# Performance work log

Measured on AMD Instinct MI355X. Metric: run time of the kernel, lower is better.

## Reference

```python
import jax, jax.numpy as jnp
import numpy as np

# Static problem dims (match input_specs / init_kwargs)
B, NQ, C, H = 2, 900, 256, 8
HGT, WID = 64, 64            # single-scale feature map (input_spatial_shapes = [[64, 64]])
N = HGT * WID                # 4096 keys
DH = C // H                  # head dim 32
RPE_HID = 512
STRIDE = 16                  # feature_stride


def setup_inputs() -> dict:
    key = jax.random.key(0)
    ks = jax.random.split(key, 24)
    p = lambda k, shape: jax.random.normal(k, shape, jnp.float32) * 0.02
    # reference boxes (cx, cy, w, h) in pixel coords of a 1024x1024 image
    ref = jax.random.uniform(ks[0], (B, NQ, 1, 4), jnp.float32)
    ref = jnp.concatenate([ref[..., :2] * (WID * STRIDE), ref[..., 2:] * 128.0], axis=-1)
    return {
        "vggt_features": jnp.zeros((1,), jnp.float32),  # unused by forward (kept for signature fidelity)
        "query": jax.random.normal(ks[1], (B, NQ, C), jnp.float32),
        "reference_2d": ref,
        "k_input_flatten": jax.random.normal(ks[2], (B, N, C), jnp.float32),
        "v_input_flatten": jax.random.normal(ks[3], (B, N, C), jnp.float32),
        "input_spatial_shapes": jnp.array([[HGT, WID]], jnp.int32),
        "input_padding_mask": jnp.zeros((B, N), jnp.bool_),
        # cpb_mlp1 (x) and cpb_mlp2 (y): Linear(2,512)+ReLU+Linear(512,H,no bias); stored as [in,out]
        "W1x": p(ks[4], (2, RPE_HID)), "b1x": jnp.zeros((RPE_HID,), jnp.float32), "W2x": p(ks[5], (RPE_HID, H)),
        "W1y": p(ks[6], (2, RPE_HID)), "b1y": jnp.zeros((RPE_HID,), jnp.float32), "W2y": p(ks[7], (RPE_HID, H)),
        "Wq": p(ks[8], (C, C)), "bq": jnp.zeros((C,), jnp.float32),
        "Wk": p(ks[9], (C, C)), "bk": jnp.zeros((C,), jnp.float32),
        "Wv": p(ks[10], (C, C)), "bv": jnp.zeros((C,), jnp.float32),
        "Wp": p(ks[11], (C, C)), "bp": jnp.zeros((C,), jnp.float32),
    }


def _mlp(d, W1, b1, W2):
    return jax.nn.relu(d @ W1 + b1) @ W2


def reference(vggt_features, query, reference_2d, k_input_flatten, v_input_flatten,
              input_spatial_shapes, input_padding_mask,
              W1x, b1x, W2x, W1y, b1y, W2y, Wq, bq, Wk, bk, Wv, bv, Wp, bp):
    h, w = HGT, WID  # static (input_spatial_shapes[0] == [HGT, WID])
    scale = DH ** -0.5
    # cxcywh -> xyxy: [B, NQ, 1, 4]
    xyxy = jnp.concatenate([reference_2d[..., :2] - reference_2d[..., 2:] / 2,
                            reference_2d[..., :2] + reference_2d[..., 2:] / 2], axis=-1)
    # pixel-center grid coords (linspace(0.5, w-0.5, w) * stride)
    pos_x = ((jnp.arange(w, dtype=jnp.float32) + 0.5) * STRIDE)[None, None, :, None]
    pos_y = ((jnp.arange(h, dtype=jnp.float32) + 0.5) * STRIDE)[None, None, :, None]
    delta_x = xyxy[..., 0::2] - pos_x  # [B, NQ, w, 2]  (x1, x2 rel. to columns)
    delta_y = xyxy[..., 1::2] - pos_y  # [B, NQ, h, 2]  (y1, y2 rel. to rows)
    rpe_x = _mlp(delta_x, W1x, b1x, W2x)  # [B, NQ, w, H]
    rpe_y = _mlp(delta_y, W1y, b1y, W2y)  # [B, NQ, h, H]
    # broadcast add over (row, col) then flatten spatial -> [B, H, NQ, N]
    rpe = (rpe_x[:, :, None] + rpe_y[:, :, :, None]).reshape(B, NQ, h * w, H).transpose(0, 3, 1, 2)
    q = (query @ Wq + bq).reshape(B, NQ, H, DH).transpose(0, 2, 1, 3) * scale  # [B,H,NQ,DH]
    k = (k_input_flatten @ Wk + bk).reshape(B, N, H, DH).transpose(0, 2, 1, 3)  # [B,H,N,DH]
    v = (v_input_flatten @ Wv + bv).reshape(B, N, H, DH).transpose(0, 2, 1, 3)  # [B,H,N,DH]
    attn = jnp.einsum('bhqd,bhkd->bhqk', q, k) + rpe
    attn = attn + input_padding_mask[:, None, None, :].astype(attn.dtype) * (-100.0)
    # torch.clip_ to finfo(min,max) is an identity on finite values; softmax follows
    attn = jax.nn.softmax(attn, axis=-1)
    x = jnp.einsum('bhqk,bhkd->bhqd', attn, v).transpose(0, 2, 1, 3).reshape(B, NQ, C)
    return x @ Wp + bp
```

## Files before the change

### kernel.cpp

```cpp
#include <hip/hip_runtime.h>
#include <hip/hip_bf16.h>
#include <cmath>

#define B_ 2
#define NQ_ 900
#define N_ 4096
#define LOG2E 1.4426950408889634f

typedef __attribute__((ext_vector_type(4))) float f32x4;
typedef __attribute__((ext_vector_type(8))) short s16x8;
typedef __attribute__((ext_vector_type(8))) _Float16 f16x8;

__device__ inline short f2bf(float x) {
    union { __hip_bfloat16 b; short s; } u;
    u.b = __float2bfloat16(x);
    return u.s;
}
__device__ inline short f2h(float x) {
    _Float16 h = (_Float16)x;
    return __builtin_bit_cast(short, h);
}

template <int CTRL>
__device__ inline float dppf(float x) {
    int xi = __builtin_bit_cast(int, x);
    int r = __builtin_amdgcn_update_dpp(xi, xi, CTRL, 0xF, 0xF, true);
    return __builtin_bit_cast(float, r);
}
__device__ inline float rowmax16(float v) {
    v = fmaxf(v, dppf<0x121>(v));
    v = fmaxf(v, dppf<0x122>(v));
    v = fmaxf(v, dppf<0x124>(v));
    v = fmaxf(v, dppf<0x128>(v));
    return v;
}
__device__ inline float rowsum16(float v) {
    v += dppf<0x121>(v);
    v += dppf<0x122>(v);
    v += dppf<0x124>(v);
    v += dppf<0x128>(v);
    return v;
}

__global__ __launch_bounds__(256) void stage1_kernel(
    const float* __restrict__ query, const float* __restrict__ kin,
    const float* __restrict__ vin,
    const float* __restrict__ Wq, const float* __restrict__ Wk,
    const float* __restrict__ Wv,
    const float* __restrict__ bqv, const float* __restrict__ bkv,
    const float* __restrict__ bvv,
    unsigned short* __restrict__ qbf, unsigned short* __restrict__ kbf,
    unsigned short* __restrict__ vbf, float qscale,
    const float* __restrict__ ref2d,
    const float* __restrict__ W1x, const float* __restrict__ b1x,
    const float* __restrict__ W1y, const float* __restrict__ b1y,
    const float* __restrict__ W2x, const float* __restrict__ W2y,
    float* __restrict__ rpe_x, float* __restrict__ rpe_y)
{
    __shared__ uint4 smem[2560];
    const int bx = blockIdx.x;
    const int tid = threadIdx.x;
    const int w = tid >> 6, l = tid & 63, quad = l >> 4, l15 = l & 15;

    if (bx < 285) {
        short* Bb = (short*)smem;
        const int mtx = bx < 29 ? 0 : (bx < 157 ? 1 : 2);
        const int tile = bx - (mtx == 0 ? 0 : mtx == 1 ? 29 : 157);
        const int m0 = tile * 64;
        const float* X = mtx == 0 ? query : mtx == 1 ? kin : vin;
        const float* W = mtx == 0 ? Wq : mtx == 1 ? Wk : Wv;
        const float* bias = mtx == 0 ? bqv : mtx == 1 ? bkv : bvv;
        unsigned short* Y = mtx == 0 ? qbf : mtx == 1 ? kbf : vbf;
        const int M = mtx == 0 ? 1800 : 8192;
        const float alpha = mtx == 0 ? qscale : 1.0f;
        const int rows_per_b = mtx == 0 ? 900 : 4096;
        const int ROWS = mtx == 0 ? 960 : 4096;
        const int wq = tid & 3, mm = tid >> 2;

        s16x8 afr[8];
        {
            const int arow = m0 + w * 16 + l15;
            const bool avalid = arow < M;
            const float* xr = X + (size_t)arow * 256;
            #pragma unroll
            for (int kc = 0; kc < 8; ++kc) {
                float4 a0 = make_float4(0.f, 0.f, 0.f, 0.f), a1 = a0;
                if (avalid) {
                    a0 = *(const float4*)(xr + kc * 32 + quad * 8);
                    a1 = *(const float4*)(xr + kc * 32 + quad * 8 + 4);
                }
                unsigned pk0 = (unsigned)(unsigned short)f2bf(a0.x) | ((unsigned)(unsigned short)f2bf(a0.y) << 16);
                unsigned pk1 = (unsigned)(unsigned short)f2bf(a0.z) | ((unsigned)(unsigned short)f2bf(a0.w) << 16);
                unsigned pk2 = (unsigned)(unsigned short)f2bf(a1.x) | ((unsigned)(unsigned short)f2bf(a1.y) << 16);
                unsigned pk3 = (unsigned)(unsigned short)f2bf(a1.z) | ((unsigned)(unsigned short)f2bf(a1.w) << 16);
                uint4 pk = make_uint4(pk0, pk1, pk2, pk3);
                afr[kc] = __builtin_bit_cast(s16x8, pk);
            }
        }

        for (int nt0 = 0; nt0 < 4; ++nt0) {
            const int n0 = nt0 * 64;
            {
                const float* wcol = W + n0 + mm;
                #pragma unroll
                for (int it = 0; it < 8; ++it) {
                    int g2 = it * 4 + wq;
                    uint4 wk4;
                    wk4.x = (unsigned)(unsigned short)f2bf(wcol[(g2 * 8 + 0) * 256])
                          | ((unsigned)(unsigned short)f2bf(wcol[(g2 * 8 + 1) * 256]) << 16);
                    wk4.y = (unsigned)(unsigned short)f2bf(wcol[(g2 * 8 + 2) * 256])
                          | ((unsigned)(unsigned short)f2bf(wcol[(g2 * 8 + 3) * 256]) << 16);
                    wk4.z = (unsigned)(unsigned short)f2bf(wcol[(g2 * 8 + 4) * 256])
                          | ((unsigned)(unsigned short)f2bf(wcol[(g2 * 8 + 5) * 256]) << 16);
                    wk4.w = (unsigned)(unsigned short)f2bf(wcol[(g2 * 8 + 6) * 256])
                          | ((unsigned)(unsigned short)f2bf(wcol[(g2 * 8 + 7) * 256]) << 16);
                    *(uint4*)(Bb + (it * 256 + mm * 4 + wq) * 8) = wk4;
                }
            }
            __syncthreads();

            f32x4 acc[4] = {{0.f,0.f,0.f,0.f},{0.f,0.f,0.f,0.f},{0.f,0.f,0.f,0.f},{0.f,0.f,0.f,0.f}};
            #pragma unroll
            for (int kc = 0; kc < 8; ++kc) {
                #pragma unroll
                for (int nt = 0; nt < 4; ++nt) {
                    s16x8 bf = *(const s16x8*)(Bb + (kc * 256 + (nt * 16 + l15) * 4 + quad) * 8);
                    acc[nt] = __builtin_amdgcn_mfma_f32_16x16x32_bf16(afr[kc], bf, acc[nt], 0, 0, 0);
                }
            }

            #pragma unroll
            for (int nt = 0; nt < 4; ++nt) {
                int n = n0 + nt * 16 + l15;
                float bs = bias[n];
                int h = n >> 5, d = n & 31;
                #pragma unroll
                for (int r = 0; r < 4; ++r) {
                    int row = m0 + w * 16 + quad * 4 + r;
                    if (row < M) {
                        int b = row / rows_per_b;
                        int pos = row - b * rows_per_b;
                        Y[((size_t)(b * 8 + h) * ROWS + pos) * 32 + d] =
                            (unsigned short)f2bf((acc[nt][r] + bs) * alpha);
                    }
                }
            }
            __syncthreads();
        }
    } else {
        short* sw2h = (short*)smem;
        short* sw2l = (short*)smem + 8192;
        float4* sUV = (float4*)(smem + 2048);
        const int bq0 = (bx - 285) * 4;

        for (int i = tid; i < 8192; i += 256) {
            int g = i >> 3, j = i & 7;
            int kcg = g >> 6, rr = g & 63, n = rr >> 2, q4 = rr & 3;
            int k = kcg * 32 + q4 * 8 + j;
            float val = ((n < 8) ? W2x[k * 8 + n] : W2y[k * 8 + (n - 8)]) * LOG2E;
            _Float16 hi = (_Float16)val;
            sw2h[i] = __builtin_bit_cast(short, hi);
            sw2l[i] = f2h(val - (float)hi);
        }

        const int k0 = tid, k1 = tid + 256;
        const float w1x0a = W1x[k0], w1x1a = W1x[512 + k0];
        const float w1y0a = W1y[k0], w1y1a = W1y[512 + k0];
        const float bxa = b1x[k0], bya = b1y[k0];
        const float vxa = -(w1x0a + w1x1a), vya = -(w1y0a + w1y1a);
        const float w1x0b = W1x[k1], w1x1b = W1x[512 + k1];
        const float w1y0b = W1y[k1], w1y1b = W1y[512 + k1];
        const float bxb = b1x[k1], byb = b1y[k1];
        const float vxb = -(w1x0b + w1x1b), vyb = -(w1y0b + w1y1b);

        const int wrow = w;
        const int row = wrow * 16 + l15;
        const float pc = (row + 0.5f) * 16.0f;

        for (int qi = 0; qi < 4; ++qi) {
            const int bq = bq0 + qi;
            {
                const float4 bb = *(const float4*)(ref2d + (size_t)bq * 4);
                float x1 = bb.x - bb.z * 0.5f, x2 = bb.x + bb.z * 0.5f;
                float y1 = bb.y - bb.w * 0.5f, y2 = bb.y + bb.w * 0.5f;
                sUV[k0] = make_float4(fmaf(w1x0a, x1, fmaf(w1x1a, x2, bxa)), vxa,
                                      fmaf(w1y0a, y1, fmaf(w1y1a, y2, bya)), vya);
                sUV[k1] = make_float4(fmaf(w1x0b, x1, fmaf(w1x1b, x2, bxb)), vxb,
                                      fmaf(w1y0b, y1, fmaf(w1y1b, y2, byb)), vyb);
            }
            __syncthreads();

            f32x4 accx = {0.f, 0.f, 0.f, 0.f}, accy = {0.f, 0.f, 0.f, 0.f};
            for (int kc = 0; kc < 16; ++kc) {
                f16x8 axh, axl, ayh, ayl;
                #pragma unroll
                for (int i = 0; i < 8; ++i) {
                    float4 u = sUV[kc * 32 + quad * 8 + i];
                    float hx = fmaxf(fmaf(u.y, pc, u.x), 0.f);
                    float hy = fmaxf(fmaf(u.w, pc, u.z), 0.f);
                    _Float16 xh = (_Float16)hx;
                    _Float16 yh = (_Float16)hy;
                    axh[i] = xh;
                    axl[i] = (_Float16)(hx - (float)xh);
                    ayh[i] = yh;
                    ayl[i] = (_Float16)(hy - (float)yh);
                }
                f16x8 bh = *(const f16x8*)(sw2h + (kc * 64 + l15 * 4 + quad) * 8);
                f16x8 bl = *(const f16x8*)(sw2l + (kc * 64 + l15 * 4 + quad) * 8);
                accx = __builtin_amdgcn_mfma_f32_16x16x32_f16(axh, bh, accx, 0, 0, 0);
                accx = __builtin_amdgcn_mfma_f32_16x16x32_f16(axh, bl, accx, 0, 0, 0);
                accx = __builtin_amdgcn_mfma_f32_16x16x32_f16(axl, bh, accx, 0, 0, 0);
                accy = __builtin_amdgcn_mfma_f32_16x16x32_f16(ayh, bh, accy, 0, 0, 0);
                accy = __builtin_amdgcn_mfma_f32_16x16x32_f16(ayh, bl, accy, 0, 0, 0);
                accy = __builtin_amdgcn_mfma_f32_16x16x32_f16(ayl, bh, accy, 0, 0, 0);
            }

            #pragma unroll
            for (int rr = 0; rr < 4; ++rr) {
                int row_out = wrow * 16 + quad * 4 + rr;
                if (l15 < 8) rpe_x[((size_t)l15 * 1800 + bq) * 64 + row_out] = accx[rr];
                else         rpe_y[((size_t)(l15 - 8) * 1800 + bq) * 64 + row_out] = accy[rr];
            }
            __syncthreads();
        }
    }
}

__global__ __launch_bounds__(256) void outproj_kernel(
    const float* __restrict__ X, const float* __restrict__ W,
    const float* __restrict__ bias, float* __restrict__ Y, int M)
{
    __shared__ short Abh[4096], Abl[4096], Bbh[4096], Bbl[4096];
    const int tid = threadIdx.x;
    const int m0 = blockIdx.x * 64, n0 = blockIdx.y * 64;
    const int w = tid >> 6, l = tid & 63, quad = l >> 4, l15 = l & 15;
    const int wq = tid & 3, mm = tid >> 2;
    const bool valid = (m0 + mm) < M;
    const float* xr = X + (size_t)(m0 + mm) * 256;
    const float* wcol = W + n0 + mm;

    f32x4 acc[4] = {{0.f,0.f,0.f,0.f},{0.f,0.f,0.f,0.f},{0.f,0.f,0.f,0.f},{0.f,0.f,0.f,0.f}};

    for (int kq = 0; kq < 4; ++kq) {
        #pragma unroll
        for (int it = 0; it < 2; ++it) {
            int g2 = it * 4 + wq;
            int kbase = kq * 64 + g2 * 8;
            float av[8], bv[8];
            #pragma unroll
            for (int j = 0; j < 8; ++j) {
                av[j] = valid ? xr[kbase + j] : 0.f;
                bv[j] = wcol[(kbase + j) * 256];
            }
            uint4 ah, al, bh, bl;
            unsigned* ahp = (unsigned*)&ah; unsigned* alp = (unsigned*)&al;
            unsigned* bhp = (unsigned*)&bh; unsigned* blp = (unsigned*)&bl;
            #pragma unroll
            for (int j2 = 0; j2 < 4; ++j2) {
                _Float16 h0 = (_Float16)av[j2 * 2], h1 = (_Float16)av[j2 * 2 + 1];
                ahp[j2] = (unsigned)(unsigned short)__builtin_bit_cast(short, h0)
                        | ((unsigned)(unsigned short)__builtin_bit_cast(short, h1) << 16);
                alp[j2] = (unsigned)(unsigned short)f2h(av[j2 * 2] - (float)h0)
                        | ((unsigned)(unsigned short)f2h(av[j2 * 2 + 1] - (float)h1) << 16);
                _Float16 g0 = (_Float16)bv[j2 * 2], g1 = (_Float16)bv[j2 * 2 + 1];
                bhp[j2] = (unsigned)(unsigned short)__builtin_bit_cast(short, g0)
                        | ((unsigned)(unsigned short)__builtin_bit_cast(short, g1) << 16);
                blp[j2] = (unsigned)(unsigned short)f2h(bv[j2 * 2] - (float)g0)
                        | ((unsigned)(unsigned short)f2h(bv[j2 * 2 + 1] - (float)g1) << 16);
            }
            int gi = (it * 256 + mm * 4 + wq) * 8;
            *(uint4*)(Abh + gi) = ah;
            *(uint4*)(Abl + gi) = al;
            *(uint4*)(Bbh + gi) = bh;
            *(uint4*)(Bbl + gi) = bl;
        }
        __syncthreads();

        #pragma unroll
        for (int kc = 0; kc < 2; ++kc) {
            int ga = (kc * 256 + (w * 16 + l15) * 4 + quad) * 8;
            f16x8 ah = *(const f16x8*)(Abh + ga);
            f16x8 al = *(const f16x8*)(Abl + ga);
            #pragma unroll
            for (int nt = 0; nt < 4; ++nt) {
                int gb = (kc * 256 + (nt * 16 + l15) * 4 + quad) * 8;
                f16x8 bh = *(const f16x8*)(Bbh + gb);
                f16x8 bl = *(const f16x8*)(Bbl + gb);
                acc[nt] = __builtin_amdgcn_mfma_f32_16x16x32_f16(ah, bh, acc[nt], 0, 0, 0);
                acc[nt] = __builtin_amdgcn_mfma_f32_16x16x32_f16(ah, bl, acc[nt], 0, 0, 0);
                acc[nt] = __builtin_amdgcn_mfma_f32_16x16x32_f16(al, bh, acc[nt], 0, 0, 0);
            }
        }
        __syncthreads();
    }

    #pragma unroll
    for (int nt = 0; nt < 4; ++nt) {
        int n = n0 + nt * 16 + l15;
        float bs = bias[n];
        #pragma unroll
        for (int r = 0; r < 4; ++r) {
            int row = m0 + w * 16 + quad * 4 + r;
            if (row < M)
                Y[(size_t)row * 256 + n] = acc[nt][r] + bs;
        }
    }
}

__global__ __launch_bounds__(512, 4) void attn_mfma_kernel(
    const unsigned short* __restrict__ qb16, const unsigned short* __restrict__ kb16,
    const unsigned short* __restrict__ vb16,
    const float* __restrict__ rpe_x, const float* __restrict__ rpe_y,
    const unsigned char* __restrict__ mask, float* __restrict__ xout)
{
    __shared__ short skf[4 * 2048];
    __shared__ short svt[4 * 2048];
    __shared__ short spb[8 * 544];
    __shared__ float ry[32 * 65];
    __shared__ unsigned long long smaskb[64];
    __shared__ float sm[8][16], sl[8][16], sLf[32];

    const int tid = threadIdx.x;
    const int qb = blockIdx.x, h = blockIdx.y, b = blockIdx.z;
    const int q0 = qb * 32;
    const int w = tid >> 6, l = tid & 63;
    const int qsub = w >> 2, g = w & 3;
    const int quad = l >> 4, l15 = l & 15;

    const unsigned short* qg = qb16 + (size_t)(b * 8 + h) * 960 * 32;
    const unsigned short* kg = kb16 + (size_t)(b * 8 + h) * 4096 * 32;
    const unsigned short* vg = vb16 + (size_t)(b * 8 + h) * 4096 * 32;
    const float* rxh = rpe_x + ((size_t)h * 1800 + b * NQ_) * 64;
    const float* ryh = rpe_y + ((size_t)h * 1800 + b * NQ_) * 64;

    for (int i = tid; i < 2048; i += 512) {
        int qq = q0 + (i >> 6), pos = i & 63;
        float vy = 0.f;
        if (qq < NQ_)
            vy = ryh[(size_t)qq * 64 + pos];
        ry[(i >> 6) * 65 + pos] = vy;
    }
    #pragma unroll
    for (int j = 0; j < 8; ++j) {
        int c = w * 8 + j;
        unsigned long long bits = __ballot(mask[(size_t)b * N_ + c * 64 + l] != 0);
        if (l == 0) smaskb[c] = bits;
    }

    s16x8 qa = *(const s16x8*)(qg + (size_t)(q0 + qsub * 16 + l15) * 32 + quad * 8);

    f32x4 rx4[4];
    #pragma unroll
    for (int t = 0; t < 4; ++t)
        #pragma unroll
        for (int r = 0; r < 4; ++r) {
            int qq = q0 + qsub * 16 + quad * 4 + r;
            rx4[t][r] = (qq < NQ_) ? rxh[(size_t)qq * 64 + t * 16 + l15] : 0.f;
        }

    const int sg = tid >> 7, role = (tid >> 6) & 1, stl = tid & 63;
    int eoff[4];
    if (role == 0) {
        #pragma unroll
        for (int t = 0; t < 4; ++t)
            eoff[t] = (t * 16 + (stl & 15)) * 32 + (stl >> 4) * 8;
    } else {
        #pragma unroll
        for (int t = 0; t < 4; ++t)
            eoff[t] = stl * 32 + t * 8;
    }
    const unsigned short* src = role ? vg : kg;

    uint4 pf[4];
    {
        size_t cb = (size_t)(sg * 16) * 2048;
        #pragma unroll
        for (int t = 0; t < 4; ++t) pf[t] = *(const uint4*)(src + cb + eoff[t]);
    }

    float mrow[4] = {-INFINITY, -INFINITY, -INFINITY, -INFINITY};
    float lrow[4] = {0.f, 0.f, 0.f, 0.f};
    f32x4 acc0 = {0.f, 0.f, 0.f, 0.f}, acc1 = {0.f, 0.f, 0.f, 0.f};
    short* pw = spb + w * 544;

    for (int i = 0; i < 16; ++i) {
        __syncthreads();
        if (role == 0) {
            #pragma unroll
            for (int t = 0; t < 4; ++t)
                *(uint4*)(skf + sg * 2048 + (t * 64 + stl) * 8) = pf[t];
        } else {
            short* vtw = svt + sg * 2048;
            #pragma unroll
            for (int t = 0; t < 4; ++t) {
                const unsigned short* pv = (const unsigned short*)&pf[t];
                #pragma unroll
                for (int j = 0; j < 8; ++j) {
                    int d = t * 8 + j;
                    vtw[d * 64 + (((stl >> 3) ^ (d & 7)) << 3) + (stl & 7)] = (short)pv[j];
                }
            }
        }
        __syncthreads();

        {
            int inext = (i + 1 < 16) ? i + 1 : 15;
            size_t cb = (size_t)(sg * 16 + inext) * 2048;
            #pragma unroll
            for (int t = 0; t < 4; ++t) pf[t] = *(const uint4*)(src + cb + eoff[t]);
        }

        const int cgc = g * 16 + i;
        const short* kf = skf + g * 2048;

        f32x4 sc[4];
        #pragma unroll
        for (int t = 0; t < 4; ++t) {
            s16x8 kb = *(const s16x8*)(kf + (t * 64 + l) * 8);
            sc[t] = __builtin_amdgcn_mfma_f32_16x16x32_bf16(qa, kb, rx4[t], 0, 0, 0);
        }
        float ryv[4];
        #pragma unroll
        for (int r = 0; r < 4; ++r)
            ryv[r] = ry[(qsub * 16 + quad * 4 + r) * 65 + cgc];
        unsigned long long mb = smaskb[cgc];
        if (mb) {
            #pragma unroll
            for (int t = 0; t < 4; ++t) {
                float mk = ((mb >> (t * 16 + l15)) & 1ULL) ? -144.2695f : 0.f;
                #pragma unroll
                for (int r = 0; r < 4; ++r) sc[t][r] += mk;
            }
        }

        float cmr[4];
        #pragma unroll
        for (int r = 0; r < 4; ++r)
            cmr[r] = fmaxf(fmaxf(sc[0][r], sc[1][r]), fmaxf(sc[2][r], sc[3][r])) + ryv[r];

        int ok = (cmr[0] <= mrow[0] + 8.f) & (cmr[1] <= mrow[1] + 8.f)
               & (cmr[2] <= mrow[2] + 8.f) & (cmr[3] <= mrow[3] + 8.f);
        if (!__all(ok)) {
            #pragma unroll
            for (int r = 0; r < 4; ++r) {
                float cm = rowmax16(cmr[r]);
                float mnew = fmaxf(mrow[r], cm);
                float al = exp2f(mrow[r] - mnew);
                mrow[r] = mnew;
                lrow[r] *= al;
                acc0[r] *= al;
                acc1[r] *= al;
            }
        }

        float msub[4];
        #pragma unroll
        for (int r = 0; r < 4; ++r) msub[r] = mrow[r] - ryv[r];
        #pragma unroll
        for (int t = 0; t < 4; ++t)
            #pragma unroll
            for (int r = 0; r < 4; ++r)
                sc[t][r] = exp2f(sc[t][r] - msub[r]);
        #pragma unroll
        for (int r = 0; r < 4; ++r)
            lrow[r] += (sc[0][r] + sc[1][r]) + (sc[2][r] + sc[3][r]);

        const short* vt = svt + g * 2048;
        #pragma unroll
        for (int hh = 0; hh < 2; ++hh) {
            #pragma unroll
            for (int tt = 0; tt < 2; ++tt) {
                int t = hh * 2 + tt;
                int gphys = (tt * 2 + (l15 >> 3)) ^ quad;
                #pragma unroll
                for (int r = 0; r < 4; ++r)
                    pw[(gphys * 17 + quad * 4 + r) * 8 + (l15 & 7)] = f2bf(sc[t][r]);
            }
            int gph_r = quad ^ (l15 >> 2);
            s16x8 pa  = *(const s16x8*)(pw + (gph_r * 17 + l15) * 8);
            int ksw = ((hh * 4 + quad) ^ (l15 & 7)) * 8;
            s16x8 vb0 = *(const s16x8*)(vt + l15 * 64 + ksw);
            s16x8 vb1 = *(const s16x8*)(vt + (16 + l15) * 64 + ksw);
            acc0 = __builtin_amdgcn_mfma_f32_16x16x32_bf16(pa, vb0, acc0, 0, 0, 0);
            acc1 = __builtin_amdgcn_mfma_f32_16x16x32_bf16(pa, vb1, acc1, 0, 0, 0);
        }
    }

    #pragma unroll
    for (int r = 0; r < 4; ++r) lrow[r] = rowsum16(lrow[r]);

    __syncthreads();
    if (l15 == 0) {
        #pragma unroll
        for (int r = 0; r < 4; ++r) {
            sm[w][quad * 4 + r] = mrow[r];
            sl[w][quad * 4 + r] = lrow[r];
        }
    }
    __syncthreads();
    float wgt[4], L4[4];
    #pragma unroll
    for (int r = 0; r < 4; ++r) {
        int qrow = quad * 4 + r;
        float mm = -INFINITY;
        #pragma unroll
        for (int gg = 0; gg < 4; ++gg) mm = fmaxf(mm, sm[qsub * 4 + gg][qrow]);
        float LL = 0.f;
        #pragma unroll
        for (int gg = 0; gg < 4; ++gg)
            LL += exp2f(sm[qsub * 4 + gg][qrow] - mm) * sl[qsub * 4 + gg][qrow];
        wgt[r] = exp2f(mrow[r] - mm);
        L4[r] = LL;
    }
    if (g == 0 && l15 == 0) {
        #pragma unroll
        for (int r = 0; r < 4; ++r) sLf[qsub * 16 + quad * 4 + r] = L4[r];
    }

    float* obuf = (float*)skf;
    for (int gg = 0; gg < 4; ++gg) {
        if (g == gg) {
            #pragma unroll
            for (int r = 0; r < 4; ++r) {
                int idx = (qsub * 16 + quad * 4 + r) * 33 + l15;
                float v0 = wgt[r] * acc0[r];
                float v1 = wgt[r] * acc1[r];
                if (gg == 0) { obuf[idx] = v0; obuf[idx + 16] = v1; }
                else         { obuf[idx] += v0; obuf[idx + 16] += v1; }
            }
        }
        __syncthreads();
    }

    for (int i = tid; i < 1024; i += 512) {
        int ql = i >> 5, d = i & 31;
        int qq = q0 + ql;
        if (qq < NQ_)
            xout[(size_t)(b * NQ_ + qq) * 256 + h * 32 + d] = obuf[ql * 33 + d] / sLf[ql];
    }
}

extern "C" void kernel_launch(void* const* d_in, const int* in_sizes, int n_in,
                              void* d_out, int out_size, void* d_ws, size_t ws_size,
                              hipStream_t stream)
{
    const float* query = (const float*)d_in[1];
    const float* ref2d = (const float*)d_in[2];
    const float* kin   = (const float*)d_in[3];
    const float* vin   = (const float*)d_in[4];
    const unsigned char* mask = (const unsigned char*)d_in[6];
    const float* W1x = (const float*)d_in[7];
    const float* b1x = (const float*)d_in[8];
    const float* W2x = (const float*)d_in[9];
    const float* W1y = (const float*)d_in[10];
    const float* b1y = (const float*)d_in[11];
    const float* W2y = (const float*)d_in[12];
    const float* Wq  = (const float*)d_in[13];
    const float* bq  = (const float*)d_in[14];
    const float* Wk  = (const float*)d_in[15];
    const float* bk  = (const float*)d_in[16];
    const float* Wv  = (const float*)d_in[17];
    const float* bv  = (const float*)d_in[18];
    const float* Wp  = (const float*)d_in[19];
    const float* bp  = (const float*)d_in[20];

    char* wsb = (char*)d_ws;
    unsigned short* qbf = (unsigned short*)(wsb);
    unsigned short* kbf = (unsigned short*)(wsb +   983040);
    unsigned short* vbf = (unsigned short*)(wsb +  5177344);
    float* rxws = (float*)(wsb +  9371648);
    float* ryws = (float*)(wsb + 13058048);
    float* xws  = (float*)(wsb + 16744448);
    float* out  = (float*)d_out;

    const float qscale = LOG2E / sqrtf(32.0f);

    stage1_kernel<<<735, 256, 0, stream>>>(
        query, kin, vin, Wq, Wk, Wv, bq, bk, bv, qbf, kbf, vbf, qscale,
        ref2d, W1x, b1x, W1y, b1y, W2x, W2y, rxws, ryws);
    attn_mfma_kernel<<<dim3(29, 8, B_), 512, 0, stream>>>(
        qbf, kbf, vbf, rxws, ryws, mask, xws);
    outproj_kernel<<<dim3(29, 4), 256, 0, stream>>>(xws, Wp, bp, out, 1800);
}
```

Measured before the change: 203.9 us.

## Pre-split and transpose Wp in stage1, stream fp16 pairs directly in outproj

Stage1 gains 16 extra blocks that convert Wp into transposed fp16 hi/lo arrays in workspace. The output projection then drops its LDS staging and per-block conversion: each lane loads its A fragments straight from X into registers and reads B fragments straight from the pre-split weights. This removes redundant weight conversion across blocks, strided column loads and barriers from outproj. In exchange it uses more registers and uncached global fragment reads, and outproj is a small share of the total time.

```diff
diff --git a/kernel.cpp b/kernel.cpp
--- a/kernel.cpp
+++ b/kernel.cpp
@@ -46,7 +46,7 @@
     const float* __restrict__ query, const float* __restrict__ kin,
     const float* __restrict__ vin,
     const float* __restrict__ Wq, const float* __restrict__ Wk,
-    const float* __restrict__ Wv,
+    const float* __restrict__ Wv, const float* __restrict__ Wp,
     const float* __restrict__ bqv, const float* __restrict__ bkv,
     const float* __restrict__ bvv,
     unsigned short* __restrict__ qbf, unsigned short* __restrict__ kbf,
@@ -55,7 +55,8 @@
     const float* __restrict__ W1x, const float* __restrict__ b1x,
     const float* __restrict__ W1y, const float* __restrict__ b1y,
     const float* __restrict__ W2x, const float* __restrict__ W2y,
-    float* __restrict__ rpe_x, float* __restrict__ rpe_y)
+    float* __restrict__ rpe_x, float* __restrict__ rpe_y,
+    unsigned short* __restrict__ wph, unsigned short* __restrict__ wpl)
 {
     __shared__ uint4 smem[2560];
     const int bx = blockIdx.x;
@@ -147,7 +148,7 @@
             }
             __syncthreads();
         }
-    } else {
+    } else if (bx < 735) {
         short* sw2h = (short*)smem;
         short* sw2l = (short*)smem + 8192;
         float4* sUV = (float4*)(smem + 2048);
@@ -223,75 +224,83 @@
             }
             __syncthreads();
         }
+    } else {
+        const int tile = bx - 735;
+        const int kt = tile >> 2, ntile = tile & 3;
+        unsigned short* th = (unsigned short*)smem;
+        unsigned short* tl = th + 64 * 72;
+        #pragma unroll
+        for (int p = 0; p < 4; ++p) {
+            int kl = p * 16 + (tid >> 4);
+            int nl = (tid & 15) * 4;
+            float4 v = *(const float4*)(Wp + (size_t)(kt * 64 + kl) * 256 + ntile * 64 + nl);
+            float vv[4] = {v.x, v.y, v.z, v.w};
+            #pragma unroll
+            for (int i = 0; i < 4; ++i) {
+                _Float16 h = (_Float16)vv[i];
+                th[(nl + i) * 72 + kl] = (unsigned short)__builtin_bit_cast(short, h);
+                tl[(nl + i) * 72 + kl] = (unsigned short)f2h(vv[i] - (float)h);
+            }
+        }
+        __syncthreads();
+        #pragma unroll
+        for (int p = 0; p < 2; ++p) {
+            int nl = p * 32 + (tid >> 3);
+            int k8 = (tid & 7) * 8;
+            uint4 pk;
+            unsigned short* ps = (unsigned short*)&pk;
+            #pragma unroll
+            for (int j = 0; j < 8; ++j) ps[j] = th[nl * 72 + k8 + j];
+            *(uint4*)(wph + (size_t)(ntile * 64 + nl) * 256 + kt * 64 + k8) = pk;
+            #pragma unroll
+            for (int j = 0; j < 8; ++j) ps[j] = tl[nl * 72 + k8 + j];
+            *(uint4*)(wpl + (size_t)(ntile * 64 + nl) * 256 + kt * 64 + k8) = pk;
+        }
     }
 }
 
 __global__ __launch_bounds__(256) void outproj_kernel(
-    const float* __restrict__ X, const float* __restrict__ W,
+    const float* __restrict__ X,
+    const unsigned short* __restrict__ wph, const unsigned short* __restrict__ wpl,
     const float* __restrict__ bias, float* __restrict__ Y, int M)
 {
-    __shared__ short Abh[4096], Abl[4096], Bbh[4096], Bbl[4096];
     const int tid = threadIdx.x;
     const int m0 = blockIdx.x * 64, n0 = blockIdx.y * 64;
     const int w = tid >> 6, l = tid & 63, quad = l >> 4, l15 = l & 15;
-    const int wq = tid & 3, mm = tid >> 2;
-    const bool valid = (m0 + mm) < M;
-    const float* xr = X + (size_t)(m0 + mm) * 256;
-    const float* wcol = W + n0 + mm;
+
+    const int arow = m0 + w * 16 + l15;
+    const bool avalid = arow < M;
+    const float* xr = X + (size_t)arow * 256;
+
+    f16x8 ah[8], al[8];
+    #pragma unroll
+    for (int kc = 0; kc < 8; ++kc) {
+        float4 a0 = make_float4(0.f, 0.f, 0.f, 0.f), a1 = a0;
+        if (avalid) {
+            a0 = *(const float4*)(xr + kc * 32 + quad * 8);
+            a1 = *(const float4*)(xr + kc * 32 + quad * 8 + 4);
+        }
+        float av[8] = {a0.x, a0.y, a0.z, a0.w, a1.x, a1.y, a1.z, a1.w};
+        #pragma unroll
+        for (int j = 0; j < 8; ++j) {
+            _Float16 h = (_Float16)av[j];
+            ah[kc][j] = h;
+            al[kc][j] = (_Float16)(av[j] - (float)h);
+        }
+    }
 
     f32x4 acc[4] = {{0.f,0.f,0.f,0.f},{0.f,0.f,0.f,0.f},{0.f,0.f,0.f,0.f},{0.f,0.f,0.f,0.f}};
-
-    for (int kq = 0; kq < 4; ++kq) {
-        #pragma unroll
-        for (int it = 0; it < 2; ++it) {
-            int g2 = it * 4 + wq;
-            int kbase = kq * 64 + g2 * 8;
-            float av[8], bv[8];
-            #pragma unroll
-            for (int j = 0; j < 8; ++j) {
-                av[j] = valid ? xr[kbase + j] : 0.f;
-                bv[j] = wcol[(kbase + j) * 256];
-            }
-            uint4 ah, al, bh, bl;
-            unsigned* ahp = (unsigned*)&ah; unsigned* alp = (unsigned*)&al;
-            unsigned* bhp = (unsigned*)&bh; unsigned* blp = (unsigned*)&bl;
-            #pragma unroll
-            for (int j2 = 0; j2 < 4; ++j2) {
-                _Float16 h0 = (_Float16)av[j2 * 2], h1 = (_Float16)av[j2 * 2 + 1];
-                ahp[j2] = (unsigned)(unsigned short)__builtin_bit_cast(short, h0)
-                        | ((unsigned)(unsigned short)__builtin_bit_cast(short, h1) << 16);
-                alp[j2] = (unsigned)(unsigned short)f2h(av[j2 * 2] - (float)h0)
-                        | ((unsigned)(unsigned short)f2h(av[j2 * 2 + 1] - (float)h1) << 16);
-                _Float16 g0 = (_Float16)bv[j2 * 2], g1 = (_Float16)bv[j2 * 2 + 1];
-                bhp[j2] = (unsigned)(unsigned short)__builtin_bit_cast(short, g0)
-                        | ((unsigned)(unsigned short)__builtin_bit_cast(short, g1) << 16);
-                blp[j2] = (unsigned)(unsigned short)f2h(bv[j2 * 2] - (float)g0)
-                        | ((unsigned)(unsigned short)f2h(bv[j2 * 2 + 1] - (float)g1) << 16);
-            }
-            int gi = (it * 256 + mm * 4 + wq) * 8;
-            *(uint4*)(Abh + gi) = ah;
-            *(uint4*)(Abl + gi) = al;
-            *(uint4*)(Bbh + gi) = bh;
-            *(uint4*)(Bbl + gi) = bl;
-        }
-        __syncthreads();
-
-        #pragma unroll
-        for (int kc = 0; kc < 2; ++kc) {
-            int ga = (kc * 256 + (w * 16 + l15) * 4 + quad) * 8;
-            f16x8 ah = *(const f16x8*)(Abh + ga);
-            f16x8 al = *(const f16x8*)(Abl + ga);
-            #pragma unroll
-            for (int nt = 0; nt < 4; ++nt) {
-                int gb = (kc * 256 + (nt * 16 + l15) * 4 + quad) * 8;
-                f16x8 bh = *(const f16x8*)(Bbh + gb);
-                f16x8 bl = *(const f16x8*)(Bbl + gb);
-                acc[nt] = __builtin_amdgcn_mfma_f32_16x16x32_f16(ah, bh, acc[nt], 0, 0, 0);
-                acc[nt] = __builtin_amdgcn_mfma_f32_16x16x32_f16(ah, bl, acc[nt], 0, 0, 0);
-                acc[nt] = __builtin_amdgcn_mfma_f32_16x16x32_f16(al, bh, acc[nt], 0, 0, 0);
-            }
-        }
-        __syncthreads();
+    #pragma unroll
+    for (int kc = 0; kc < 8; ++kc) {
+        #pragma unroll
+        for (int nt = 0; nt < 4; ++nt) {
+            size_t gb = (size_t)(n0 + nt * 16 + l15) * 256 + kc * 32 + quad * 8;
+            f16x8 bh = *(const f16x8*)(wph + gb);
+            f16x8 bl = *(const f16x8*)(wpl + gb);
+            acc[nt] = __builtin_amdgcn_mfma_f32_16x16x32_f16(ah[kc], bh, acc[nt], 0, 0, 0);
+            acc[nt] = __builtin_amdgcn_mfma_f32_16x16x32_f16(ah[kc], bl, acc[nt], 0, 0, 0);
+            acc[nt] = __builtin_amdgcn_mfma_f32_16x16x32_f16(al[kc], bh, acc[nt], 0, 0, 0);
+        }
     }
 
     #pragma unroll
@@ -571,14 +580,17 @@
     float* rxws = (float*)(wsb +  9371648);
     float* ryws = (float*)(wsb + 13058048);
     float* xws  = (float*)(wsb + 16744448);
+    unsigned short* wph = (unsigned short*)(wsb + 18587648);
+    unsigned short* wpl = (unsigned short*)(wsb + 18718720);
     float* out  = (float*)d_out;
 
     const float qscale = LOG2E / sqrtf(32.0f);
 
-    stage1_kernel<<<735, 256, 0, stream>>>(
-        query, kin, vin, Wq, Wk, Wv, bq, bk, bv, qbf, kbf, vbf, qscale,
-        ref2d, W1x, b1x, W1y, b1y, W2x, W2y, rxws, ryws);
+    stage1_kernel<<<751, 256, 0, stream>>>(
+        query, kin, vin, Wq, Wk, Wv, Wp, bq, bk, bv, qbf, kbf, vbf, qscale,
+        ref2d, W1x, b1x, W1y, b1y, W2x, W2y, rxws, ryws, wph, wpl);
     attn_mfma_kernel<<<dim3(29, 8, B_), 512, 0, stream>>>(
         qbf, kbf, vbf, rxws, ryws, mask, xws);
-    outproj_kernel<<<dim3(29, 4), 256, 0, stream>>>(xws, Wp, bp, out, 1800);
-}
+    outproj_kernel<<<dim3(29, 4), 256, 0, stream>>>(
+        xws, wph, wpl, bp, out, 1800);
+}
```

Result: no change. 200.4 us (median of 2 runs) (-1.7%).
